# Performance work log

Hardware: AMD Instinct MI355X
Metric: run time of the kernel (lower is better)

Reference implementation:

```python
import jax, jax.numpy as jnp
import numpy as np
import math

B, LQ, LK = 4, 1024, 2048
QD, KD, VD = 768, 512, 512
H, NH = 1024, 16
HD = H // NH

def setup_inputs() -> dict:
    key = jax.random.key(0)
    ks = jax.random.split(key, 11)
    s = 0.02
    return {
        "query": jax.random.normal(ks[0], (B, LQ, QD), jnp.float32),
        "key": jax.random.normal(ks[1], (B, LK, KD), jnp.float32),
        "value": jax.random.normal(ks[2], (B, LK, VD), jnp.float32),
        "Wq": jax.random.normal(ks[3], (QD, H), jnp.float32) * s,
        "bq": jnp.zeros((H,), jnp.float32),
        "Wk": jax.random.normal(ks[4], (KD, H), jnp.float32) * s,
        "bk": jnp.zeros((H,), jnp.float32),
        "Wv": jax.random.normal(ks[5], (VD, H), jnp.float32) * s,
        "bv": jnp.zeros((H,), jnp.float32),
        "Wo": jax.random.normal(ks[6], (H, H), jnp.float32) * s,
        "bo": jnp.zeros((H,), jnp.float32),
    }

def reference(query, key, value, Wq, bq, Wk, bk, Wv, bv, Wo, bo):
    # project and split heads: [B, L, H] -> [B, NH, L, HD]
    def heads(x):
        b, l, _ = x.shape
        return x.reshape(b, l, NH, HD).transpose(0, 2, 1, 3)
    q = heads(query @ Wq + bq)   # [B, NH, LQ, HD]
    k = heads(key @ Wk + bk)     # [B, NH, LK, HD]
    v = heads(value @ Wv + bv)   # [B, NH, LK, HD]
    scores = jnp.einsum('bhqd,bhkd->bhqk', q, k) / math.sqrt(HD)
    weights = jax.nn.softmax(scores, axis=-1)  # dropout inactive (eval / rate used deterministically as identity)
    att = jnp.einsum('bhqk,bhkd->bhqd', weights, v)
    att = att.transpose(0, 2, 1, 3).reshape(query.shape[0], -1, H)
    out = att @ Wo + bo
    return out
```

## Files before the change

### kernel.cpp

```cpp
#include <hip/hip_runtime.h>
#include <math.h>

using bf16x8 = __attribute__((ext_vector_type(8))) short;
using f32x4  = __attribute__((ext_vector_type(4))) float;
using u32x2  = __attribute__((ext_vector_type(2))) unsigned int;

namespace {
constexpr int kB  = 4;
constexpr int kLQ = 1024;
constexpr int kLK = 2048;
constexpr int kH  = 1024;
constexpr int kHD = 64;
}

__device__ __forceinline__ unsigned short f2bf(float x) {
  union { float f; unsigned int u; } v; v.f = x;
  unsigned int r = v.u + 0x7fffu + ((v.u >> 16) & 1u);
  return (unsigned short)(r >> 16);
}

typedef const __attribute__((address_space(1))) unsigned int guint_t;
typedef __attribute__((address_space(3))) unsigned int luint_t;
__device__ __forceinline__ void g2l16(const void* g, void* l) {
  __builtin_amdgcn_global_load_lds(
      (guint_t*)g,
      (luint_t*)(unsigned int)(unsigned long long)l,
      16, 0, 0);
}

__global__ __launch_bounds__(256) void prep_kernel(
    const float* __restrict__ q, const float* __restrict__ k,
    const float* __restrict__ v, const float* __restrict__ Wq,
    const float* __restrict__ Wk, const float* __restrict__ Wv,
    const float* __restrict__ Wo, unsigned short* __restrict__ qo,
    unsigned short* __restrict__ ko, unsigned short* __restrict__ vo,
    unsigned short* __restrict__ WqT, unsigned short* __restrict__ WkT,
    unsigned short* __restrict__ WvT, unsigned short* __restrict__ WoT)
{
  __shared__ float tile[64][65];
  const int t = threadIdx.x;
  if (blockIdx.x < 5632) {
    int c = blockIdx.x * 256 + t;
    const float* src; unsigned short* dst;
    if (c < 393216)      { src = q; dst = qo; }
    else if (c < 917504) { src = k; dst = ko; c -= 393216; }
    else                 { src = v; dst = vo; c -= 917504; }
    const int i = c * 8;
    const float4 a = *(const float4*)(src + i);
    const float4 b = *(const float4*)(src + i + 4);
    uint4 o;
    o.x = (unsigned int)f2bf(a.x) | ((unsigned int)f2bf(a.y) << 16);
    o.y = (unsigned int)f2bf(a.z) | ((unsigned int)f2bf(a.w) << 16);
    o.z = (unsigned int)f2bf(b.x) | ((unsigned int)f2bf(b.y) << 16);
    o.w = (unsigned int)f2bf(b.z) | ((unsigned int)f2bf(b.w) << 16);
    *(uint4*)(dst + i) = o;
    return;
  }
  int id = blockIdx.x - 5632;
  const float* W; unsigned short* Wt; int Kd;
  if (id < 192)      { W = Wq; Wt = WqT; Kd = 768; }
  else if (id < 320) { W = Wk; Wt = WkT; Kd = 512;  id -= 192; }
  else if (id < 448) { W = Wv; Wt = WvT; Kd = 512;  id -= 320; }
  else               { W = Wo; Wt = WoT; Kd = 1024; id -= 448; }
  const int Nd = 1024;
  const int n0 = (id & 15) * 64;
  const int k0 = (id >> 4) * 64;
  const int rr = t >> 4;
  const int c4 = t & 15;
#pragma unroll
  for (int i = 0; i < 4; ++i) {
    const int row = i * 16 + rr;
    const float4 vv = *(const float4*)(W + (size_t)(k0 + row) * Nd + n0 + c4 * 4);
    tile[row][c4*4+0] = vv.x; tile[row][c4*4+1] = vv.y;
    tile[row][c4*4+2] = vv.z; tile[row][c4*4+3] = vv.w;
  }
  __syncthreads();
#pragma unroll
  for (int i = 0; i < 4; ++i) {
    const int n = i * 16 + rr;
    ushort4 o;
    o.x = f2bf(tile[c4*4+0][n]); o.y = f2bf(tile[c4*4+1][n]);
    o.z = f2bf(tile[c4*4+2][n]); o.w = f2bf(tile[c4*4+3][n]);
    *(ushort4*)(Wt + (size_t)(n0 + n) * Kd + k0 + c4 * 4) = o;
  }
}

__device__ __forceinline__ void gemm_body(
    const unsigned short* __restrict__ A, const unsigned short* __restrict__ Bt,
    const float* __restrict__ bias, void* __restrict__ Cout,
    int N, int K, int bx, int by, int mode, float scale, char* lds)
{
  const int t    = threadIdx.x;
  const int lane = t & 63;
  const int w    = t >> 6;
  const int l15  = lane & 15;
  const int lq8  = (lane >> 4) * 8;
  const int lq4  = (lane >> 4) * 4;
  const int r0   = by * 128;
  const int c0   = bx * 128;
  const int wm   = w >> 1, wn = w & 1;

  f32x4 acc[4][4] = {};

  const unsigned short* gsrc[4];
  char* ldst[4];
#pragma unroll
  for (int i = 0; i < 4; ++i) {
    const int g = w * 4 + i;
    const unsigned short* src = (g < 8) ? A : Bt;
    const int rbase = (g < 8) ? (r0 + g * 16) : (c0 + (g - 8) * 16);
    gsrc[i] = src + (size_t)(rbase + l15) * K + lq8;
    ldst[i] = lds + g * 1024 + lane * 16;
  }

#pragma unroll
  for (int i = 0; i < 4; ++i) g2l16(gsrc[i], ldst[i]);
#pragma unroll
  for (int i = 0; i < 4; ++i) g2l16(gsrc[i] + 32, ldst[i] + 16384);

  int slot = 0;
  for (int k0 = 0; k0 < K; k0 += 32) {
    if (k0 + 32 < K) {
      asm volatile("s_waitcnt vmcnt(4)\n\ts_barrier" ::: "memory");
    } else {
      asm volatile("s_waitcnt vmcnt(0)\n\ts_barrier" ::: "memory");
    }
    char* buf = lds + slot * 16384;
    if (k0 + 64 < K) {
      int ns = slot + 2; if (ns >= 3) ns -= 3;
#pragma unroll
      for (int i = 0; i < 4; ++i)
        g2l16(gsrc[i] + k0 + 64, ldst[i] + ns * 16384);
    }
    bf16x8 af[4], bfr[4];
#pragma unroll
    for (int i = 0; i < 4; ++i) af[i]  = *(const bf16x8*)(buf + (wm*4 + i) * 1024 + lane * 16);
#pragma unroll
    for (int j = 0; j < 4; ++j) bfr[j] = *(const bf16x8*)(buf + 8192 + (wn*4 + j) * 1024 + lane * 16);
#pragma unroll
    for (int i = 0; i < 4; ++i)
#pragma unroll
      for (int j = 0; j < 4; ++j)
        acc[i][j] = (mode == 2)
          ? __builtin_amdgcn_mfma_f32_16x16x32_bf16(af[i], bfr[j], acc[i][j], 0, 0, 0)
          : __builtin_amdgcn_mfma_f32_16x16x32_bf16(bfr[j], af[i], acc[i][j], 0, 0, 0);
    slot = (slot == 2) ? 0 : slot + 1;
  }

  if (mode == 2) {
#pragma unroll
    for (int j = 0; j < 4; ++j) {
      const int col = c0 + wn * 64 + j * 16 + l15;
      const float bcol = bias[col];
#pragma unroll
      for (int i = 0; i < 4; ++i) {
        const int row = r0 + wm * 64 + i * 16 + lq4;
        unsigned short* out = (unsigned short*)Cout;
        const int bb = row >> 11;
        const int lk = row & 2047;
        ushort4 o;
        o.x = f2bf(acc[i][j][0] + bcol); o.y = f2bf(acc[i][j][1] + bcol);
        o.z = f2bf(acc[i][j][2] + bcol); o.w = f2bf(acc[i][j][3] + bcol);
        *(ushort4*)(out + (size_t)(bb * kH + col) * kLK + lk) = o;
      }
    }
  } else {
#pragma unroll
    for (int i = 0; i < 4; ++i) {
      const int row = r0 + wm * 64 + i * 16 + l15;
#pragma unroll
      for (int j = 0; j < 4; ++j) {
        const int ncol = c0 + wn * 64 + j * 16 + lq4;
        const float4 b4 = *(const float4*)(bias + ncol);
        if (mode == 0) {
          float4 o;
          o.x = acc[i][j][0] + b4.x; o.y = acc[i][j][1] + b4.y;
          o.z = acc[i][j][2] + b4.z; o.w = acc[i][j][3] + b4.w;
          *(float4*)((float*)Cout + (size_t)row * N + ncol) = o;
        } else {
          ushort4 o;
          o.x = f2bf((acc[i][j][0] + b4.x) * scale);
          o.y = f2bf((acc[i][j][1] + b4.y) * scale);
          o.z = f2bf((acc[i][j][2] + b4.z) * scale);
          o.w = f2bf((acc[i][j][3] + b4.w) * scale);
          *(ushort4*)((unsigned short*)Cout + (size_t)row * N + ncol) = o;
        }
      }
    }
  }
}

__global__ __launch_bounds__(256) void qkv_gemm_kernel(
    const unsigned short* __restrict__ qA, const unsigned short* __restrict__ WqT,
    const float* __restrict__ bq, unsigned short* __restrict__ Qb,
    const unsigned short* __restrict__ kA, const unsigned short* __restrict__ WkT,
    const float* __restrict__ bk, unsigned short* __restrict__ Kb,
    const unsigned short* __restrict__ vA, const unsigned short* __restrict__ WvT,
    const float* __restrict__ bv, unsigned short* __restrict__ Vtw)
{
  __shared__ __align__(16) char lds[49152];
  int id = blockIdx.x;
  if (id < 256) {
    gemm_body(qA, WqT, bq, Qb, 1024, 768, id & 7, id >> 3, 1,
              0.18033688011112042f, lds);
  } else if (id < 768) {
    id -= 256;
    gemm_body(kA, WkT, bk, Kb, 1024, 512, id & 7, id >> 3, 1, 1.f, lds);
  } else {
    id -= 768;
    gemm_body(vA, WvT, bv, Vtw, 1024, 512, id & 7, id >> 3, 2, 1.f, lds);
  }
}

__global__ __launch_bounds__(256) void out_gemm_kernel(
    const unsigned short* __restrict__ A, const unsigned short* __restrict__ Bt,
    const float* __restrict__ bias, float* __restrict__ C)
{
  __shared__ __align__(16) char lds[49152];
  const int id = blockIdx.x;
  gemm_body(A, Bt, bias, C, 1024, 1024, id & 7, id >> 3, 0, 1.f, lds);
}

__global__ __launch_bounds__(256) void attn_mfma_kernel(
    const unsigned short* __restrict__ Q, const unsigned short* __restrict__ K,
    const unsigned short* __restrict__ Vt, unsigned short* __restrict__ O)
{
  __shared__ __align__(16) char lds[65536];
  constexpr int POFF = 49152;
  const int t    = threadIdx.x;
  const int lane = t & 63;
  const int w    = t >> 6;
  const int l15  = lane & 15;
  const int lg   = lane >> 4;
  const int lq8  = lg * 8;
  const int lq4  = lg * 4;
  const int flat = blockIdx.x;
  const int bh   = flat & 63;
  const int qb   = flat >> 6;
  const int h    = bh & 15;
  const int b    = bh >> 4;
  const int q0   = qb * 128;
  const int hoff = h * kHD;
  constexpr int NT = kLK / 64;

  bf16x8 qf[2][2];
#pragma unroll
  for (int qi = 0; qi < 2; ++qi)
#pragma unroll
    for (int kh = 0; kh < 2; ++kh)
      qf[qi][kh] = *(const bf16x8*)(Q + (size_t)(b*kLQ + q0 + w*32 + qi*16 + l15) * kH
                                      + hoff + kh*32 + lq8);

  f32x4 acc[2][4] = {};
  float lsum[2] = {0.f, 0.f};

  const int swz  = ((l15 * 5) & 7) << 4;
  const int colw = (lg * 8)  ^ swz;
  const int colr = (lg * 16) ^ swz;

  const unsigned short* gsrc[4];
  int gstep[4];
  char* ldst[4];
#pragma unroll
  for (int i = 0; i < 4; ++i) {
    const int g = w * 4 + i;
    if (g < 8) {
      gsrc[i]  = K + (size_t)(b*kLK + (g >> 1)*16 + l15) * kH + hoff + (g & 1)*32 + lq8;
      gstep[i] = 64 * kH;
    } else {
      const int gg = g - 8;
      gsrc[i]  = Vt + (size_t)(b*kH + hoff + (gg >> 1)*16 + l15) * kLK + (gg & 1)*32 + lq8;
      gstep[i] = 64;
    }
    ldst[i] = lds + g * 1024 + lane * 16;
  }

#pragma unroll
  for (int i = 0; i < 4; ++i) g2l16(gsrc[i], ldst[i]);
#pragma unroll
  for (int i = 0; i < 4; ++i) g2l16(gsrc[i] + gstep[i], ldst[i] + 16384);

  int slot = 0;
  for (int kt = 0; kt < NT; ++kt) {
    if (kt + 1 < NT) {
      asm volatile("s_waitcnt vmcnt(4)\n\ts_barrier" ::: "memory");
    } else {
      asm volatile("s_waitcnt vmcnt(0)\n\ts_barrier" ::: "memory");
    }
    char* buf = lds + slot * 16384;
    if (kt + 2 < NT) {
      int ns = slot + 2; if (ns >= 3) ns -= 3;
#pragma unroll
      for (int i = 0; i < 4; ++i)
        g2l16(gsrc[i] + (size_t)(kt + 2) * gstep[i], ldst[i] + ns * 16384);
    }

    f32x4 s[2][4];
#pragma unroll
    for (int kcf = 0; kcf < 4; ++kcf) {
      const bf16x8 kf0 = *(const bf16x8*)(buf + (kcf*2 + 0) * 1024 + lane * 16);
      const bf16x8 kf1 = *(const bf16x8*)(buf + (kcf*2 + 1) * 1024 + lane * 16);
#pragma unroll
      for (int qi = 0; qi < 2; ++qi) {
        f32x4 z = {};
        z = __builtin_amdgcn_mfma_f32_16x16x32_bf16(kf0, qf[qi][0], z, 0, 0, 0);
        z = __builtin_amdgcn_mfma_f32_16x16x32_bf16(kf1, qf[qi][1], z, 0, 0, 0);
        s[qi][kcf] = z;
      }
    }

#pragma unroll
    for (int qi = 0; qi < 2; ++qi) {
      char* const prow = lds + POFF + (w*32 + qi*16 + l15) * 128;
#pragma unroll
      for (int kcf = 0; kcf < 4; ++kcf) {
        const float p0 = __builtin_amdgcn_exp2f(s[qi][kcf][0]);
        const float p1 = __builtin_amdgcn_exp2f(s[qi][kcf][1]);
        const float p2 = __builtin_amdgcn_exp2f(s[qi][kcf][2]);
        const float p3 = __builtin_amdgcn_exp2f(s[qi][kcf][3]);
        lsum[qi] += (p0 + p1) + (p2 + p3);
        u32x2 pw;
        pw.x = __builtin_amdgcn_perm(__float_as_uint(p1), __float_as_uint(p0), 0x07060302u);
        pw.y = __builtin_amdgcn_perm(__float_as_uint(p3), __float_as_uint(p2), 0x07060302u);
        *(u32x2*)(prow + (colw ^ (kcf * 32))) = pw;
      }
    }

    bf16x8 pf[2][2];
#pragma unroll
    for (int qi = 0; qi < 2; ++qi) {
      const char* const prow = lds + POFF + (w*32 + qi*16 + l15) * 128;
#pragma unroll
      for (int kq = 0; kq < 2; ++kq)
        pf[qi][kq] = *(const bf16x8*)(prow + (colr ^ (kq * 64)));
    }
#pragma unroll
    for (int vd = 0; vd < 4; ++vd) {
      const bf16x8 vf0 = *(const bf16x8*)(buf + 8192 + (vd*2 + 0) * 1024 + lane * 16);
      const bf16x8 vf1 = *(const bf16x8*)(buf + 8192 + (vd*2 + 1) * 1024 + lane * 16);
#pragma unroll
      for (int qi = 0; qi < 2; ++qi) {
        acc[qi][vd] = __builtin_amdgcn_mfma_f32_16x16x32_bf16(vf0, pf[qi][0], acc[qi][vd], 0, 0, 0);
        acc[qi][vd] = __builtin_amdgcn_mfma_f32_16x16x32_bf16(vf1, pf[qi][1], acc[qi][vd], 0, 0, 0);
      }
    }
    slot = (slot == 2) ? 0 : slot + 1;
  }

  float rinv[2];
#pragma unroll
  for (int qi = 0; qi < 2; ++qi) {
    float v = lsum[qi];
    v += __shfl_xor(v, 16);
    v += __shfl_xor(v, 32);
    rinv[qi] = 1.f / v;
  }
#pragma unroll
  for (int qi = 0; qi < 2; ++qi)
#pragma unroll
    for (int vd = 0; vd < 4; ++vd) {
      ushort4 o;
      o.x = f2bf(acc[qi][vd][0] * rinv[qi]);
      o.y = f2bf(acc[qi][vd][1] * rinv[qi]);
      o.z = f2bf(acc[qi][vd][2] * rinv[qi]);
      o.w = f2bf(acc[qi][vd][3] * rinv[qi]);
      *(ushort4*)(O + (size_t)(b*kLQ + q0 + w*32 + qi*16 + l15) * kH
                    + hoff + vd*16 + lq4) = o;
    }
}

extern "C" void kernel_launch(void* const* d_in, const int* in_sizes, int n_in,
                              void* d_out, int out_size, void* d_ws, size_t ws_size,
                              hipStream_t stream) {
  (void)in_sizes; (void)n_in; (void)out_size; (void)ws_size;
  const float* query = (const float*)d_in[0];
  const float* key   = (const float*)d_in[1];
  const float* value = (const float*)d_in[2];
  const float* Wq = (const float*)d_in[3];
  const float* bq = (const float*)d_in[4];
  const float* Wk = (const float*)d_in[5];
  const float* bk = (const float*)d_in[6];
  const float* Wv = (const float*)d_in[7];
  const float* bv = (const float*)d_in[8];
  const float* Wo = (const float*)d_in[9];
  const float* bo = (const float*)d_in[10];
  float* out = (float*)d_out;

  unsigned short* ws  = (unsigned short*)d_ws;
  unsigned short* qA  = ws;
  unsigned short* kA  = qA  + 3145728;
  unsigned short* vA  = kA  + 4194304;
  unsigned short* WqT = vA  + 4194304;
  unsigned short* WkT = WqT + 786432;
  unsigned short* WvT = WkT + 524288;
  unsigned short* WoT = WvT + 524288;
  unsigned short* Qb  = WoT + 1048576;
  unsigned short* Kb  = Qb  + 4194304;
  unsigned short* Vtw = Kb  + 8388608;
  unsigned short* Ab  = Vtw + 8388608;

  prep_kernel<<<6336, 256, 0, stream>>>(query, key, value, Wq, Wk, Wv, Wo,
                                        qA, kA, vA, WqT, WkT, WvT, WoT);
  qkv_gemm_kernel<<<1280, 256, 0, stream>>>(qA, WqT, bq, Qb,
                                            kA, WkT, bk, Kb,
                                            vA, WvT, bv, Vtw);
  attn_mfma_kernel<<<512, 256, 0, stream>>>(Qb, Kb, Vtw, Ab);
  out_gemm_kernel<<<256, 256, 0, stream>>>(Ab, WoT, bo, out);
}
```

Before: 238.0 us.

## Split attention work across 8 waves with one Q tile each, double-buffer K/V

The attention kernel now launches 512 threads per block, so each of 8 waves owns 16 query rows instead of 4 waves owning 32. The K/V prefetch ring shrinks from triple to double buffering, each wave issues half as many global-to-LDS loads, and LDS use drops from 64 KB to 48 KB. The aim is more waves in flight to hide latency and fewer registers per wave. The cost is a full vmcnt(0) wait plus barrier every tile, with one tile of prefetch instead of two, which exposes more load latency.

After: 225.4 us. 5.3% less time.

```diff
diff --git a/kernel.cpp b/kernel.cpp
--- a/kernel.cpp
+++ b/kernel.cpp
@@ -221,12 +221,12 @@
   gemm_body(A, Bt, bias, C, 1024, 1024, id & 7, id >> 3, 0, 1.f, lds);
 }
 
-__global__ __launch_bounds__(256) void attn_mfma_kernel(
+__global__ __launch_bounds__(512) void attn_mfma_kernel(
     const unsigned short* __restrict__ Q, const unsigned short* __restrict__ K,
     const unsigned short* __restrict__ Vt, unsigned short* __restrict__ O)
 {
-  __shared__ __align__(16) char lds[65536];
-  constexpr int POFF = 49152;
+  __shared__ __align__(16) char lds[49152];
+  constexpr int POFF = 32768;
   const int t    = threadIdx.x;
   const int lane = t & 63;
   const int w    = t >> 6;
@@ -243,27 +243,26 @@
   const int hoff = h * kHD;
   constexpr int NT = kLK / 64;
 
-  bf16x8 qf[2][2];
-#pragma unroll
-  for (int qi = 0; qi < 2; ++qi)
-#pragma unroll
-    for (int kh = 0; kh < 2; ++kh)
-      qf[qi][kh] = *(const bf16x8*)(Q + (size_t)(b*kLQ + q0 + w*32 + qi*16 + l15) * kH
-                                      + hoff + kh*32 + lq8);
-
-  f32x4 acc[2][4] = {};
-  float lsum[2] = {0.f, 0.f};
+  bf16x8 qf[2];
+#pragma unroll
+  for (int kh = 0; kh < 2; ++kh)
+    qf[kh] = *(const bf16x8*)(Q + (size_t)(b*kLQ + q0 + w*16 + l15) * kH
+                                + hoff + kh*32 + lq8);
+
+  f32x4 acc[4] = {};
+  float lsum = 0.f;
 
   const int swz  = ((l15 * 5) & 7) << 4;
   const int colw = (lg * 8)  ^ swz;
   const int colr = (lg * 16) ^ swz;
-
-  const unsigned short* gsrc[4];
-  int gstep[4];
-  char* ldst[4];
-#pragma unroll
-  for (int i = 0; i < 4; ++i) {
-    const int g = w * 4 + i;
+  char* const prow = lds + POFF + (w*16 + l15) * 128;
+
+  const unsigned short* gsrc[2];
+  int gstep[2];
+  char* ldst[2];
+#pragma unroll
+  for (int i = 0; i < 2; ++i) {
+    const int g = w * 2 + i;
     if (g < 8) {
       gsrc[i]  = K + (size_t)(b*kLK + (g >> 1)*16 + l15) * kH + hoff + (g & 1)*32 + lq8;
       gstep[i] = 64 * kH;
@@ -275,98 +274,69 @@
     ldst[i] = lds + g * 1024 + lane * 16;
   }
 
-#pragma unroll
-  for (int i = 0; i < 4; ++i) g2l16(gsrc[i], ldst[i]);
-#pragma unroll
-  for (int i = 0; i < 4; ++i) g2l16(gsrc[i] + gstep[i], ldst[i] + 16384);
-
-  int slot = 0;
+  g2l16(gsrc[0], ldst[0]);
+  g2l16(gsrc[1], ldst[1]);
+
   for (int kt = 0; kt < NT; ++kt) {
+    asm volatile("s_waitcnt vmcnt(0)\n\ts_barrier" ::: "memory");
+    char* buf = lds + (kt & 1) * 16384;
     if (kt + 1 < NT) {
-      asm volatile("s_waitcnt vmcnt(4)\n\ts_barrier" ::: "memory");
-    } else {
-      asm volatile("s_waitcnt vmcnt(0)\n\ts_barrier" ::: "memory");
-    }
-    char* buf = lds + slot * 16384;
-    if (kt + 2 < NT) {
-      int ns = slot + 2; if (ns >= 3) ns -= 3;
-#pragma unroll
-      for (int i = 0; i < 4; ++i)
-        g2l16(gsrc[i] + (size_t)(kt + 2) * gstep[i], ldst[i] + ns * 16384);
-    }
-
-    f32x4 s[2][4];
+      const int ns = (kt + 1) & 1;
+      g2l16(gsrc[0] + (size_t)(kt + 1) * gstep[0], ldst[0] + ns * 16384);
+      g2l16(gsrc[1] + (size_t)(kt + 1) * gstep[1], ldst[1] + ns * 16384);
+    }
+
+    f32x4 s[4];
 #pragma unroll
     for (int kcf = 0; kcf < 4; ++kcf) {
       const bf16x8 kf0 = *(const bf16x8*)(buf + (kcf*2 + 0) * 1024 + lane * 16);
       const bf16x8 kf1 = *(const bf16x8*)(buf + (kcf*2 + 1) * 1024 + lane * 16);
-#pragma unroll
-      for (int qi = 0; qi < 2; ++qi) {
-        f32x4 z = {};
-        z = __builtin_amdgcn_mfma_f32_16x16x32_bf16(kf0, qf[qi][0], z, 0, 0, 0);
-        z = __builtin_amdgcn_mfma_f32_16x16x32_bf16(kf1, qf[qi][1], z, 0, 0, 0);
-        s[qi][kcf] = z;
-      }
-    }
-
-#pragma unroll
-    for (int qi = 0; qi < 2; ++qi) {
-      char* const prow = lds + POFF + (w*32 + qi*16 + l15) * 128;
-#pragma unroll
-      for (int kcf = 0; kcf < 4; ++kcf) {
-        const float p0 = __builtin_amdgcn_exp2f(s[qi][kcf][0]);
-        const float p1 = __builtin_amdgcn_exp2f(s[qi][kcf][1]);
-        const float p2 = __builtin_amdgcn_exp2f(s[qi][kcf][2]);
-        const float p3 = __builtin_amdgcn_exp2f(s[qi][kcf][3]);
-        lsum[qi] += (p0 + p1) + (p2 + p3);
-        u32x2 pw;
-        pw.x = __builtin_amdgcn_perm(__float_as_uint(p1), __float_as_uint(p0), 0x07060302u);
-        pw.y = __builtin_amdgcn_perm(__float_as_uint(p3), __float_as_uint(p2), 0x07060302u);
-        *(u32x2*)(prow + (colw ^ (kcf * 32))) = pw;
-      }
-    }
-
-    bf16x8 pf[2][2];
-#pragma unroll
-    for (int qi = 0; qi < 2; ++qi) {
-      const char* const prow = lds + POFF + (w*32 + qi*16 + l15) * 128;
-#pragma unroll
-      for (int kq = 0; kq < 2; ++kq)
-        pf[qi][kq] = *(const bf16x8*)(prow + (colr ^ (kq * 64)));
-    }
+      f32x4 z = {};
+      z = __builtin_amdgcn_mfma_f32_16x16x32_bf16(kf0, qf[0], z, 0, 0, 0);
+      z = __builtin_amdgcn_mfma_f32_16x16x32_bf16(kf1, qf[1], z, 0, 0, 0);
+      s[kcf] = z;
+    }
+
+#pragma unroll
+    for (int kcf = 0; kcf < 4; ++kcf) {
+      const float p0 = __builtin_amdgcn_exp2f(s[kcf][0]);
+      const float p1 = __builtin_amdgcn_exp2f(s[kcf][1]);
+      const float p2 = __builtin_amdgcn_exp2f(s[kcf][2]);
+      const float p3 = __builtin_amdgcn_exp2f(s[kcf][3]);
+      lsum += (p0 + p1) + (p2 + p3);
+      u32x2 pw;
+      pw.x = __builtin_amdgcn_perm(__float_as_uint(p1), __float_as_uint(p0), 0x07060302u);
+      pw.y = __builtin_amdgcn_perm(__float_as_uint(p3), __float_as_uint(p2), 0x07060302u);
+      *(u32x2*)(prow + (colw ^ (kcf * 32))) = pw;
+    }
+
+    bf16x8 pf[2];
+#pragma unroll
+    for (int kq = 0; kq < 2; ++kq)
+      pf[kq] = *(const bf16x8*)(prow + (colr ^ (kq * 64)));
 #pragma unroll
     for (int vd = 0; vd < 4; ++vd) {
       const bf16x8 vf0 = *(const bf16x8*)(buf + 8192 + (vd*2 + 0) * 1024 + lane * 16);
       const bf16x8 vf1 = *(const bf16x8*)(buf + 8192 + (vd*2 + 1) * 1024 + lane * 16);
-#pragma unroll
-      for (int qi = 0; qi < 2; ++qi) {
-        acc[qi][vd] = __builtin_amdgcn_mfma_f32_16x16x32_bf16(vf0, pf[qi][0], acc[qi][vd], 0, 0, 0);
-        acc[qi][vd] = __builtin_amdgcn_mfma_f32_16x16x32_bf16(vf1, pf[qi][1], acc[qi][vd], 0, 0, 0);
-      }
-    }
-    slot = (slot == 2) ? 0 : slot + 1;
-  }
-
-  float rinv[2];
-#pragma unroll
-  for (int qi = 0; qi < 2; ++qi) {
-    float v = lsum[qi];
-    v += __shfl_xor(v, 16);
-    v += __shfl_xor(v, 32);
-    rinv[qi] = 1.f / v;
-  }
-#pragma unroll
-  for (int qi = 0; qi < 2; ++qi)
-#pragma unroll
-    for (int vd = 0; vd < 4; ++vd) {
-      ushort4 o;
-      o.x = f2bf(acc[qi][vd][0] * rinv[qi]);
-      o.y = f2bf(acc[qi][vd][1] * rinv[qi]);
-      o.z = f2bf(acc[qi][vd][2] * rinv[qi]);
-      o.w = f2bf(acc[qi][vd][3] * rinv[qi]);
-      *(ushort4*)(O + (size_t)(b*kLQ + q0 + w*32 + qi*16 + l15) * kH
-                    + hoff + vd*16 + lq4) = o;
-    }
+      acc[vd] = __builtin_amdgcn_mfma_f32_16x16x32_bf16(vf0, pf[0], acc[vd], 0, 0, 0);
+      acc[vd] = __builtin_amdgcn_mfma_f32_16x16x32_bf16(vf1, pf[1], acc[vd], 0, 0, 0);
+    }
+  }
+
+  float v = lsum;
+  v += __shfl_xor(v, 16);
+  v += __shfl_xor(v, 32);
+  const float rinv = 1.f / v;
+#pragma unroll
+  for (int vd = 0; vd < 4; ++vd) {
+    ushort4 o;
+    o.x = f2bf(acc[vd][0] * rinv);
+    o.y = f2bf(acc[vd][1] * rinv);
+    o.z = f2bf(acc[vd][2] * rinv);
+    o.w = f2bf(acc[vd][3] * rinv);
+    *(ushort4*)(O + (size_t)(b*kLQ + q0 + w*16 + l15) * kH
+                  + hoff + vd*16 + lq4) = o;
+  }
 }
 
 extern "C" void kernel_launch(void* const* d_in, const int* in_sizes, int n_in,
@@ -404,6 +374,6 @@
   qkv_gemm_kernel<<<1280, 256, 0, stream>>>(qA, WqT, bq, Qb,
                                             kA, WkT, bk, Kb,
                                             vA, WvT, bv, Vtw);
-  attn_mfma_kernel<<<512, 256, 0, stream>>>(Qb, Kb, Vtw, Ab);
+  attn_mfma_kernel<<<512, 512, 0, stream>>>(Qb, Kb, Vtw, Ab);
   out_gemm_kernel<<<256, 256, 0, stream>>>(Ab, WoT, bo, out);
 }
```
